# Kernel tuning notes

Hardware: AMD Instinct MI355X
Metric: run time of the kernel (lower is better)

Reference implementation:

```python
import math
import jax, jax.numpy as jnp
import numpy as np

B, S, D, H = 4, 1024, 1024, 16
DK = D // H
NEG = jnp.float32(-1e32)
EPS = 1e-5


def setup_inputs() -> dict:
    key = jax.random.key(0)
    ks = jax.random.split(key, 10)
    s = 1.0 / math.sqrt(D)
    return {
        "query": jax.random.normal(ks[0], (B, S, D), jnp.float32),
        "key": jax.random.normal(ks[1], (B, S, D), jnp.float32),
        "values": jax.random.normal(ks[2], (B, S, D), jnp.float32),
        "lens": jax.random.randint(ks[3], (B,), 0, S).astype(jnp.int32),
        "state_weight": jax.random.normal(ks[4], (1, H, S, S), jnp.float32),
        # params (kq_same=True -> k shares q_linear weights)
        "Wq": jax.random.normal(ks[5], (D, D), jnp.float32) * s,
        "bq": jnp.zeros((D,), jnp.float32),
        "Wv": jax.random.normal(ks[6], (D, D), jnp.float32) * s,
        "bv": jnp.zeros((D,), jnp.float32),
        "Wo": jax.random.normal(ks[7], (D, D), jnp.float32) * s,
        "bo": jnp.zeros((D,), jnp.float32),
        "gamma": jnp.ones((D,), jnp.float32),
        "beta": jnp.zeros((D,), jnp.float32),
    }


def reference(query, key, values, lens, state_weight, Wq, bq, Wv, bv, Wo, bo, gamma, beta):
    # eval-mode forward of DTransformerLayer (peek_cur=False -> strictly causal)
    b, s, d = query.shape
    mask = jnp.tril(jnp.ones((s, s), bool), -1)[None, None]  # [1,1,S,S]

    q = (query @ Wq + bq).reshape(b, s, H, DK).transpose(0, 2, 1, 3)   # bhsd
    k = (key @ Wq + bq).reshape(b, s, H, DK).transpose(0, 2, 1, 3)     # shared weights (kq_same)
    v = (values @ Wv + bv).reshape(b, s, H, DK).transpose(0, 2, 1, 3)

    scores = jnp.einsum('bhqd,bhkd->bhqk', q, k) / math.sqrt(DK)
    scores = jnp.where(mask, scores, NEG)
    scores = jnp.where(mask, scores + state_weight, NEG)
    attn = jax.nn.softmax(scores, axis=-1)
    attn = jnp.where(mask, attn, 0.0)  # fully-masked rows (row 0) -> zeros, matching torch

    ctx = jnp.einsum('bhqk,bhkd->bhqd', attn, v).transpose(0, 2, 1, 3).reshape(b, s, d)
    out = ctx @ Wo + bo

    x = query + out  # dropout is identity in eval
    mu = jnp.mean(x, axis=-1, keepdims=True)
    var = jnp.mean(jnp.square(x - mu), axis=-1, keepdims=True)
    return (x - mu) * jax.lax.rsqrt(var + EPS) * gamma + beta
```

## Files before the change

kernel.cpp:

```cpp
#include <hip/hip_runtime.h>

#define B_ 4
#define S_ 1024
#define D_ 1024
#define H_ 16
#define DK_ 64

typedef __attribute__((ext_vector_type(8))) short short8;
typedef __attribute__((ext_vector_type(4))) float f32x4;
typedef __attribute__((ext_vector_type(16))) float f32x16;

static __device__ __forceinline__ unsigned bf16rne(float x) {
    unsigned b = __float_as_uint(x);
    return (b + 0x7FFFu + ((b >> 16) & 1u)) >> 16;
}

__global__ __launch_bounds__(256) void cvt3_bf16(
    const float* __restrict__ q, const float* __restrict__ k,
    const float* __restrict__ v, ushort* __restrict__ out)
{
    const size_t i = ((size_t)blockIdx.x * 256 + threadIdx.x) * 8;
    const size_t FM = (size_t)4 * 1024 * 1024;
    const float* in = (i < FM) ? q : (i < 2 * FM) ? k : v;
    const size_t off = i & (FM - 1);
    const float4 a = *reinterpret_cast<const float4*>(in + off);
    const float4 b = *reinterpret_cast<const float4*>(in + off + 4);
    union { ushort u[8]; int4 vv; } p;
    p.u[0] = (ushort)bf16rne(a.x); p.u[1] = (ushort)bf16rne(a.y);
    p.u[2] = (ushort)bf16rne(a.z); p.u[3] = (ushort)bf16rne(a.w);
    p.u[4] = (ushort)bf16rne(b.x); p.u[5] = (ushort)bf16rne(b.y);
    p.u[6] = (ushort)bf16rne(b.z); p.u[7] = (ushort)bf16rne(b.w);
    *reinterpret_cast<int4*>(out + i) = p.vv;
}

__global__ __launch_bounds__(256) void transpose_cvt3(
    const float* __restrict__ W0, const float* __restrict__ W1,
    const float* __restrict__ W2, ushort* __restrict__ T0,
    ushort* __restrict__ T1, ushort* __restrict__ T2)
{
    __shared__ float ts[32][33];
    const float* W = (blockIdx.z == 0) ? W0 : (blockIdx.z == 1) ? W1 : W2;
    ushort*     Wt = (blockIdx.z == 0) ? T0 : (blockIdx.z == 1) ? T1 : T2;
    const int t  = threadIdx.x;
    const int k0 = blockIdx.y * 32, n0 = blockIdx.x * 32;
    const int r  = t >> 3, c4 = (t & 7) * 4;
    const float4 v = *reinterpret_cast<const float4*>(&W[(size_t)(k0 + r) * 1024 + n0 + c4]);
    ts[r][c4] = v.x; ts[r][c4 + 1] = v.y; ts[r][c4 + 2] = v.z; ts[r][c4 + 3] = v.w;
    __syncthreads();
    ushort4 o;
    o.x = (ushort)bf16rne(ts[c4    ][r]);
    o.y = (ushort)bf16rne(ts[c4 + 1][r]);
    o.z = (ushort)bf16rne(ts[c4 + 2][r]);
    o.w = (ushort)bf16rne(ts[c4 + 3][r]);
    *reinterpret_cast<ushort4*>(&Wt[(size_t)(n0 + r) * 1024 + k0 + c4]) = o;
}

template<int MODE>
__global__ __launch_bounds__(256) void gemm_mfma(
    const ushort* __restrict__ X, const ushort* __restrict__ Wt,
    const float* __restrict__ bias, const float* __restrict__ resid,
    void* __restrict__ out0, void* __restrict__ out1)
{
    __shared__ ushort As[64 * 64];
    __shared__ ushort Bs[128 * 64];

    const int t    = threadIdx.x;
    const int lane = t & 63;
    const int w    = t >> 6;

    const int cpx     = gridDim.x >> 3;
    const int logical = (blockIdx.x & 7) * cpx + (blockIdx.x >> 3);
    const int bm = logical >> 3;
    const int bn = logical & 7;

    const int srow   = lane >> 3;
    const int schunk = (lane & 7) ^ srow;
    const ushort* ag[2];
    const ushort* bg[4];
#pragma unroll
    for (int j = 0; j < 2; ++j)
        ag[j] = X  + (size_t)(bm * 64 + (j * 4 + w) * 8 + srow) * 1024 + schunk * 8;
#pragma unroll
    for (int j = 0; j < 4; ++j)
        bg[j] = Wt + (size_t)(bn * 128 + (j * 4 + w) * 8 + srow) * 1024 + schunk * 8;

#define STAGE(k0)                                                                \
    do {                                                                         \
        _Pragma("unroll")                                                        \
        for (int j = 0; j < 2; ++j)                                              \
            __builtin_amdgcn_global_load_lds(                                    \
                (__attribute__((address_space(1))) const void*)(ag[j] + (k0)),   \
                (__attribute__((address_space(3))) void*)&As[(j * 4 + w) * 512], \
                16, 0, 0);                                                       \
        _Pragma("unroll")                                                        \
        for (int j = 0; j < 4; ++j)                                              \
            __builtin_amdgcn_global_load_lds(                                    \
                (__attribute__((address_space(1))) const void*)(bg[j] + (k0)),   \
                (__attribute__((address_space(3))) void*)&Bs[(j * 4 + w) * 512], \
                16, 0, 0);                                                       \
    } while (0)

    const int fr = lane & 15;
    const int fk = lane >> 4;
    const int wm = w >> 1, wn = w & 1;

    f32x4 acc[2][4];
#pragma unroll
    for (int m = 0; m < 2; ++m)
#pragma unroll
        for (int n = 0; n < 4; ++n) acc[m][n] = (f32x4){0.f, 0.f, 0.f, 0.f};

#pragma unroll 1
    for (int kt = 0; kt < 16; ++kt) {
        STAGE(kt * 64);
        __syncthreads();
#pragma unroll
        for (int ks = 0; ks < 2; ++ks) {
            short8 af[2], bf[4];
#pragma unroll
            for (int m = 0; m < 2; ++m) {
                const int row = wm * 32 + m * 16 + fr;
                af[m] = *reinterpret_cast<const short8*>(
                    &As[row * 64 + (((ks * 4 + fk) ^ (row & 7)) * 8)]);
            }
#pragma unroll
            for (int n = 0; n < 4; ++n) {
                const int row = wn * 64 + n * 16 + fr;
                bf[n] = *reinterpret_cast<const short8*>(
                    &Bs[row * 64 + (((ks * 4 + fk) ^ (row & 7)) * 8)]);
            }
#pragma unroll
            for (int m = 0; m < 2; ++m)
#pragma unroll
                for (int n = 0; n < 4; ++n)
                    acc[m][n] = __builtin_amdgcn_mfma_f32_16x16x32_bf16(
                        af[m], bf[n], acc[m][n], 0, 0, 0);
        }
        __syncthreads();
    }
#undef STAGE

#pragma unroll
    for (int m = 0; m < 2; ++m) {
        const int row0 = bm * 64 + wm * 32 + m * 16 + fk * 4;
#pragma unroll
        for (int n = 0; n < 4; ++n) {
            const int col = bn * 128 + wn * 64 + n * 16 + fr;
            const float bc = bias[col];
            if (MODE == 0) {
                float* o = (float*)out0;
#pragma unroll
                for (int j = 0; j < 4; ++j) {
                    const int row = row0 + j;
                    o[(size_t)row * 1024 + col] =
                        acc[m][n][j] + bc + resid[(size_t)row * 1024 + col];
                }
            } else if (MODE == 1) {
                ushort* o = (row0 < 4096) ? (ushort*)out0 : (ushort*)out1;
                const int r0 = row0 & 4095;
                const int b_ = r0 >> 10, s0 = r0 & 1023;
                const int h  = col >> 6,  dk = col & 63;
#pragma unroll
                for (int j = 0; j < 4; ++j)
                    o[(((size_t)b_ * H_ + h) * S_ + s0 + j) * DK_ + dk] =
                        (ushort)bf16rne(acc[m][n][j] + bc);
            } else {
                ushort* o = (ushort*)out0;
                const int b_ = row0 >> 10, s0 = row0 & 1023;
                const int h  = col >> 6,   dk = col & 63;
                ushort4 pk;
                pk.x = (ushort)bf16rne(acc[m][n][0] + bc);
                pk.y = (ushort)bf16rne(acc[m][n][1] + bc);
                pk.z = (ushort)bf16rne(acc[m][n][2] + bc);
                pk.w = (ushort)bf16rne(acc[m][n][3] + bc);
                *reinterpret_cast<ushort4*>(
                    &o[(((size_t)b_ * H_ + h) * DK_ + dk) * S_ + s0]) = pk;
            }
        }
    }
}

__global__ __launch_bounds__(256) void attn_mfma(
    const ushort* __restrict__ Qh, const ushort* __restrict__ Kh,
    const ushort* __restrict__ Vt, const float* __restrict__ SW,
    ushort* __restrict__ ctxP, float2* __restrict__ ml)
{
    __shared__ ushort Ks[2][4096];
    __shared__ ushort Vs[2][4096];

    const int t    = threadIdx.x;
    const int lane = t & 63;
    const int w    = t >> 6;
    const int bid  = blockIdx.x;
    const int bh   = bid & 63;
    const int b    = bh >> 4;
    const int h    = bh & 15;
    const int qp   = bid >> 6;
    const int p    = qp >> 3;
    int qb = qp & 7;
    qb = (qb < 4) ? qb : 11 - qb;

    const int ql = lane & 31;
    const int hi = lane >> 5;
    const int qrow = qb * 128 + ql * 4 + w;
    const int t0 = p * (qb + 1);
    const int nt = qb + 1;

    const ushort* Kg  = Kh + (size_t)bh * S_ * DK_;
    const ushort* Vg  = Vt + (size_t)bh * DK_ * S_;
    const float*  swp = SW + ((size_t)h * S_ + qrow) * S_;

    const ushort* kgp[2];
    const ushort* vgp[2];
#pragma unroll
    for (int j = 0; j < 2; ++j) {
        const int bb = w * 2 + j;
        const int g = bb >> 2, c = bb & 3;
        kgp[j] = Kg + (size_t)(g * 32 + ql) * DK_ + c * 16 + hi * 8;
        vgp[j] = Vg + (size_t)(g * 32 + ql) * S_  + c * 16 + hi * 8;
    }

#define ASTAGE(buf, k0)                                                          \
    do {                                                                         \
        _Pragma("unroll")                                                        \
        for (int j = 0; j < 2; ++j) {                                            \
            const int bb = w * 2 + j;                                            \
            __builtin_amdgcn_global_load_lds(                                    \
                (__attribute__((address_space(1))) const void*)(kgp[j] + (size_t)(k0) * DK_), \
                (__attribute__((address_space(3))) void*)&Ks[buf][bb * 512],     \
                16, 0, 0);                                                       \
            __builtin_amdgcn_global_load_lds(                                    \
                (__attribute__((address_space(1))) const void*)(vgp[j] + (k0)),  \
                (__attribute__((address_space(3))) void*)&Vs[buf][bb * 512],     \
                16, 0, 0);                                                       \
        }                                                                        \
    } while (0)

    short8 qf[4];
    {
        const ushort* Qg = Qh + ((size_t)bh * S_ + qrow) * DK_;
#pragma unroll
        for (int c = 0; c < 4; ++c) {
            union { int4 i; short8 s; } u;
            u.i = *reinterpret_cast<const int4*>(&Qg[c * 16 + hi * 8]);
            qf[c] = u.s;
        }
    }

    f32x16 accA, accB;
#pragma unroll
    for (int r = 0; r < 16; ++r) { accA[r] = 0.f; accB[r] = 0.f; }
    float mrow = -1e30f, lrow = 0.f;

    ASTAGE(0, t0 * 64);

#pragma unroll 1
    for (int kt = 0; kt < nt; ++kt) {
        const int cur = kt & 1;
        const int k0  = (t0 + kt) * 64;
        if (kt + 1 < nt) {
            ASTAGE(cur ^ 1, (t0 + kt + 1) * 64);
            asm volatile("s_waitcnt vmcnt(4)" ::: "memory");
        } else {
            asm volatile("s_waitcnt vmcnt(0)" ::: "memory");
        }
        __builtin_amdgcn_s_barrier();
        __builtin_amdgcn_sched_barrier(0);

        f32x16 sc[2];
#pragma unroll
        for (int g = 0; g < 2; ++g) {
#pragma unroll
            for (int r = 0; r < 16; ++r) sc[g][r] = 0.f;
#pragma unroll
            for (int c = 0; c < 4; ++c) {
                const short8 kf = *reinterpret_cast<const short8*>(
                    &Ks[cur][((g * 4 + c) * 64 + lane) * 8]);
                sc[g] = __builtin_amdgcn_mfma_f32_32x32x16_bf16(kf, qf[c], sc[g], 0, 0, 0);
            }
        }

        float swv[2][16];
#pragma unroll
        for (int g = 0; g < 2; ++g)
#pragma unroll
            for (int j = 0; j < 4; ++j) {
                const float4 v = *reinterpret_cast<const float4*>(
                    &swp[k0 + g * 32 + hi * 4 + j * 8]);
                swv[g][j * 4 + 0] = v.x; swv[g][j * 4 + 1] = v.y;
                swv[g][j * 4 + 2] = v.z; swv[g][j * 4 + 3] = v.w;
            }

        float pr[2][16];
        float tmax = -1e30f;
#pragma unroll
        for (int g = 0; g < 2; ++g)
#pragma unroll
            for (int r = 0; r < 16; ++r) {
                const int key = k0 + g * 32 + (r & 3) + ((r >> 2) << 3) + (hi << 2);
                const float s = (key < qrow) ? sc[g][r] * 0.125f + swv[g][r] : -1e30f;
                pr[g][r] = s;
                tmax = fmaxf(tmax, s);
            }
        tmax = fmaxf(tmax, __shfl_xor(tmax, 32, 64));
        const float mnew = fmaxf(mrow, tmax);
        const float corr = __expf(mrow - mnew);
        float psum = 0.f;
#pragma unroll
        for (int g = 0; g < 2; ++g)
#pragma unroll
            for (int r = 0; r < 16; ++r) {
                const float e = (pr[g][r] > -1e29f) ? __expf(pr[g][r] - mnew) : 0.f;
                pr[g][r] = e;
                psum += e;
            }
        psum += __shfl_xor(psum, 32, 64);
        lrow = lrow * corr + psum;
        mrow = mnew;
#pragma unroll
        for (int r = 0; r < 16; ++r) { accA[r] *= corr; accB[r] *= corr; }

        short8 paf[4];
#pragma unroll
        for (int g = 0; g < 2; ++g) {
            unsigned pk[8];
#pragma unroll
            for (int j = 0; j < 8; ++j)
                pk[j] = bf16rne(pr[g][2 * j]) | (bf16rne(pr[g][2 * j + 1]) << 16);
            unsigned x0 = (unsigned)__shfl_xor((int)pk[0], 32, 64);
            unsigned x1 = (unsigned)__shfl_xor((int)pk[1], 32, 64);
            unsigned x2 = (unsigned)__shfl_xor((int)pk[2], 32, 64);
            unsigned x3 = (unsigned)__shfl_xor((int)pk[3], 32, 64);
            unsigned x4 = (unsigned)__shfl_xor((int)pk[4], 32, 64);
            unsigned x5 = (unsigned)__shfl_xor((int)pk[5], 32, 64);
            unsigned x6 = (unsigned)__shfl_xor((int)pk[6], 32, 64);
            unsigned x7 = (unsigned)__shfl_xor((int)pk[7], 32, 64);
            union { unsigned u[4]; short8 s; } a0, a1;
            a0.u[0] = hi ? x2 : pk[0];
            a0.u[1] = hi ? x3 : pk[1];
            a0.u[2] = hi ? pk[2] : x0;
            a0.u[3] = hi ? pk[3] : x1;
            a1.u[0] = hi ? x6 : pk[4];
            a1.u[1] = hi ? x7 : pk[5];
            a1.u[2] = hi ? pk[6] : x4;
            a1.u[3] = hi ? pk[7] : x5;
            paf[g * 2 + 0] = a0.s;
            paf[g * 2 + 1] = a1.s;
        }

#pragma unroll
        for (int cc = 0; cc < 4; ++cc) {
            const short8 va = *reinterpret_cast<const short8*>(
                &Vs[cur][((0 * 4 + cc) * 64 + lane) * 8]);
            const short8 vb = *reinterpret_cast<const short8*>(
                &Vs[cur][((1 * 4 + cc) * 64 + lane) * 8]);
            accA = __builtin_amdgcn_mfma_f32_32x32x16_bf16(va, paf[cc], accA, 0, 0, 0);
            accB = __builtin_amdgcn_mfma_f32_32x32x16_bf16(vb, paf[cc], accB, 0, 0, 0);
        }

        __builtin_amdgcn_sched_barrier(0);
        __builtin_amdgcn_s_barrier();
        __builtin_amdgcn_sched_barrier(0);
    }
#undef ASTAGE

    const float inv = (lrow > 0.f) ? 1.f / lrow : 0.f;
    ushort* crow_ = ctxP + (size_t)p * 4194304 +
                    ((size_t)b * S_ + qrow) * D_ + h * DK_;
#pragma unroll
    for (int g = 0; g < 4; ++g) {
        ushort4 oA, oB;
        oA.x = (ushort)bf16rne(accA[4 * g + 0] * inv);
        oA.y = (ushort)bf16rne(accA[4 * g + 1] * inv);
        oA.z = (ushort)bf16rne(accA[4 * g + 2] * inv);
        oA.w = (ushort)bf16rne(accA[4 * g + 3] * inv);
        oB.x = (ushort)bf16rne(accB[4 * g + 0] * inv);
        oB.y = (ushort)bf16rne(accB[4 * g + 1] * inv);
        oB.z = (ushort)bf16rne(accB[4 * g + 2] * inv);
        oB.w = (ushort)bf16rne(accB[4 * g + 3] * inv);
        *reinterpret_cast<ushort4*>(&crow_[g * 8 + hi * 4])      = oA;
        *reinterpret_cast<ushort4*>(&crow_[g * 8 + hi * 4 + 32]) = oB;
    }
    if (hi == 0) {
        float2 v; v.x = mrow; v.y = lrow;
        ml[((size_t)p * 64 + bh) * 1024 + qrow] = v;
    }
}

__global__ __launch_bounds__(256) void attn_merge(
    const ushort* __restrict__ ctxP, const float2* __restrict__ ml,
    ushort* __restrict__ ctx)
{
    const size_t idx = ((size_t)blockIdx.x * 256 + threadIdx.x) * 8;
    const int col = (int)(idx & 1023);
    const int row = (int)(idx >> 10);
    const int b = row >> 10, s = row & 1023;
    const int h = col >> 6;
    const int bh = b * 16 + h;
    const float2 ml0 = ml[(size_t)bh * 1024 + s];
    const float2 ml1 = ml[(size_t)(64 + bh) * 1024 + s];
    const float m  = fmaxf(ml0.x, ml1.x);
    const float a0 = ml0.y * __expf(ml0.x - m);
    const float a1 = ml1.y * __expf(ml1.x - m);
    const float d  = a0 + a1;
    const float w0 = (d > 0.f) ? a0 / d : 0.f;
    const float w1 = (d > 0.f) ? a1 / d : 0.f;
    union { int4 v; ushort u[8]; } p0, p1, o;
    p0.v = *reinterpret_cast<const int4*>(ctxP + idx);
    p1.v = *reinterpret_cast<const int4*>(ctxP + 4194304 + idx);
#pragma unroll
    for (int i = 0; i < 8; ++i) {
        const float f0 = __uint_as_float((unsigned)p0.u[i] << 16);
        const float f1 = __uint_as_float((unsigned)p1.u[i] << 16);
        o.u[i] = (ushort)bf16rne(w0 * f0 + w1 * f1);
    }
    *reinterpret_cast<int4*>(ctx + idx) = o.v;
}

__global__ __launch_bounds__(256) void layernorm_k(
    const float* __restrict__ x, const float* __restrict__ gamma,
    const float* __restrict__ beta, float* __restrict__ out)
{
    const int row = blockIdx.x;
    const int t   = threadIdx.x;
    const float4 v = *reinterpret_cast<const float4*>(&x[(size_t)row * D_ + (t << 2)]);
    float sum = v.x + v.y + v.z + v.w;
    float sq  = v.x * v.x + v.y * v.y + v.z * v.z + v.w * v.w;
#pragma unroll
    for (int w = 1; w < 64; w <<= 1) {
        sum += __shfl_xor(sum, w, 64);
        sq  += __shfl_xor(sq,  w, 64);
    }
    __shared__ float red[8];
    const int wid = t >> 6;
    if ((t & 63) == 0) { red[wid] = sum; red[wid + 4] = sq; }
    __syncthreads();
    sum = red[0] + red[1] + red[2] + red[3];
    sq  = red[4] + red[5] + red[6] + red[7];
    const float mu  = sum * (1.f / 1024.f);
    const float var = sq * (1.f / 1024.f) - mu * mu;
    const float rs  = rsqrtf(var + 1e-5f);
    const float4 gm = *reinterpret_cast<const float4*>(&gamma[t << 2]);
    const float4 bt = *reinterpret_cast<const float4*>(&beta[t << 2]);
    float4 o;
    o.x = (v.x - mu) * rs * gm.x + bt.x;
    o.y = (v.y - mu) * rs * gm.y + bt.y;
    o.z = (v.z - mu) * rs * gm.z + bt.z;
    o.w = (v.w - mu) * rs * gm.w + bt.w;
    *reinterpret_cast<float4*>(&out[(size_t)row * D_ + (t << 2)]) = o;
}

extern "C" void kernel_launch(void* const* d_in, const int* in_sizes, int n_in,
                              void* d_out, int out_size, void* d_ws, size_t ws_size,
                              hipStream_t stream)
{
    const float* query  = (const float*)d_in[0];
    const float* key    = (const float*)d_in[1];
    const float* values = (const float*)d_in[2];
    const float* SW     = (const float*)d_in[4];
    const float* Wq     = (const float*)d_in[5];
    const float* bq     = (const float*)d_in[6];
    const float* Wv     = (const float*)d_in[7];
    const float* bv     = (const float*)d_in[8];
    const float* Wo     = (const float*)d_in[9];
    const float* bo     = (const float*)d_in[10];
    const float* gamma  = (const float*)d_in[11];
    const float* beta   = (const float*)d_in[12];

    char* ws = (char*)d_ws;
    const size_t MB = 1024 * 1024;
    ushort* qbf  = (ushort*)(ws);
    ushort* kbf  = (ushort*)(ws +  8 * MB);
    ushort* vbf  = (ushort*)(ws + 16 * MB);
    ushort* Wqt  = (ushort*)(ws + 24 * MB);
    ushort* Wvt  = (ushort*)(ws + 26 * MB);
    ushort* Wot  = (ushort*)(ws + 28 * MB);
    ushort* Qh   = (ushort*)(ws + 30 * MB);
    ushort* Kh   = (ushort*)(ws + 38 * MB);
    ushort* Vt   = (ushort*)(ws + 46 * MB);
    float2* ml   = (float2*)(ws + 54 * MB);
    ushort* ctxP = qbf;
    ushort* ctxm = vbf;
    float*  xbf  = (float*)(ws + 30 * MB);

    const dim3 blk(256);

    cvt3_bf16<<<dim3(6144), blk, 0, stream>>>(query, key, values, qbf);
    transpose_cvt3<<<dim3(32, 32, 3), blk, 0, stream>>>(Wq, Wv, Wo, Wqt, Wvt, Wot);

    gemm_mfma<1><<<dim3(1024), blk, 0, stream>>>(qbf, Wqt, bq, nullptr, Qh, Kh);
    gemm_mfma<2><<<dim3(512),  blk, 0, stream>>>(vbf, Wvt, bv, nullptr, Vt, nullptr);

    attn_mfma<<<dim3(1024), blk, 0, stream>>>(Qh, Kh, Vt, SW, ctxP, ml);
    attn_merge<<<dim3(2048), blk, 0, stream>>>(ctxP, ml, ctxm);

    gemm_mfma<0><<<dim3(512), blk, 0, stream>>>(ctxm, Wot, bo, query, xbf, nullptr);

    layernorm_k<<<dim3(4096), blk, 0, stream>>>(xbf, gamma, beta, (float*)d_out);
}
```

Before: 144.2 us.

## Double-buffer GEMM loads, rebalance attention key-splits, skip masking on interior tiles

The GEMM main loop gets double-buffered LDS staging: the next K tile loads while the current one is consumed, with explicit vmcnt waits, raw barriers, and raised wave priority around the MFMAs. Attention replaces the fixed two-way key split with variable-size chunks of up to four tiles, giving 1280 evenly sized blocks plus an XCD-aware block remap. The causal-mask compare is skipped on tiles lying entirely below the diagonal, and the probability pack uses v_cvt_pk_bf16_f32. The merge kernel now combines up to four partial results per row through a compact chunk layout, and workspace buffers are shuffled to fit.

```diff
diff --git a/kernel.cpp b/kernel.cpp
--- a/kernel.cpp
+++ b/kernel.cpp
@@ -9,6 +9,8 @@
 typedef __attribute__((ext_vector_type(8))) short short8;
 typedef __attribute__((ext_vector_type(4))) float f32x4;
 typedef __attribute__((ext_vector_type(16))) float f32x16;
+
+#define CBASE_PACK 0x100C090604020100ULL
 
 static __device__ __forceinline__ unsigned bf16rne(float x) {
     unsigned b = __float_as_uint(x);
@@ -61,8 +63,8 @@
     const float* __restrict__ bias, const float* __restrict__ resid,
     void* __restrict__ out0, void* __restrict__ out1)
 {
-    __shared__ ushort As[64 * 64];
-    __shared__ ushort Bs[128 * 64];
+    __shared__ ushort As[2][64 * 64];
+    __shared__ ushort Bs[2][128 * 64];
 
     const int t    = threadIdx.x;
     const int lane = t & 63;
@@ -84,19 +86,19 @@
     for (int j = 0; j < 4; ++j)
         bg[j] = Wt + (size_t)(bn * 128 + (j * 4 + w) * 8 + srow) * 1024 + schunk * 8;
 
-#define STAGE(k0)                                                                \
+#define STAGE(buf, k0)                                                           \
     do {                                                                         \
         _Pragma("unroll")                                                        \
         for (int j = 0; j < 2; ++j)                                              \
             __builtin_amdgcn_global_load_lds(                                    \
                 (__attribute__((address_space(1))) const void*)(ag[j] + (k0)),   \
-                (__attribute__((address_space(3))) void*)&As[(j * 4 + w) * 512], \
+                (__attribute__((address_space(3))) void*)&As[buf][(j * 4 + w) * 512], \
                 16, 0, 0);                                                       \
         _Pragma("unroll")                                                        \
         for (int j = 0; j < 4; ++j)                                              \
             __builtin_amdgcn_global_load_lds(                                    \
                 (__attribute__((address_space(1))) const void*)(bg[j] + (k0)),   \
-                (__attribute__((address_space(3))) void*)&Bs[(j * 4 + w) * 512], \
+                (__attribute__((address_space(3))) void*)&Bs[buf][(j * 4 + w) * 512], \
                 16, 0, 0);                                                       \
     } while (0)
 
@@ -110,10 +112,18 @@
 #pragma unroll
         for (int n = 0; n < 4; ++n) acc[m][n] = (f32x4){0.f, 0.f, 0.f, 0.f};
 
+    STAGE(0, 0);
 #pragma unroll 1
     for (int kt = 0; kt < 16; ++kt) {
-        STAGE(kt * 64);
-        __syncthreads();
+        const int cur = kt & 1;
+        if (kt + 1 < 16) {
+            STAGE(cur ^ 1, (kt + 1) * 64);
+            asm volatile("s_waitcnt vmcnt(6)" ::: "memory");
+        } else {
+            asm volatile("s_waitcnt vmcnt(0)" ::: "memory");
+        }
+        __builtin_amdgcn_s_barrier();
+        __builtin_amdgcn_sched_barrier(0);
 #pragma unroll
         for (int ks = 0; ks < 2; ++ks) {
             short8 af[2], bf[4];
@@ -121,22 +131,26 @@
             for (int m = 0; m < 2; ++m) {
                 const int row = wm * 32 + m * 16 + fr;
                 af[m] = *reinterpret_cast<const short8*>(
-                    &As[row * 64 + (((ks * 4 + fk) ^ (row & 7)) * 8)]);
+                    &As[cur][row * 64 + (((ks * 4 + fk) ^ (row & 7)) * 8)]);
             }
 #pragma unroll
             for (int n = 0; n < 4; ++n) {
                 const int row = wn * 64 + n * 16 + fr;
                 bf[n] = *reinterpret_cast<const short8*>(
-                    &Bs[row * 64 + (((ks * 4 + fk) ^ (row & 7)) * 8)]);
-            }
+                    &Bs[cur][row * 64 + (((ks * 4 + fk) ^ (row & 7)) * 8)]);
+            }
+            __builtin_amdgcn_s_setprio(1);
 #pragma unroll
             for (int m = 0; m < 2; ++m)
 #pragma unroll
                 for (int n = 0; n < 4; ++n)
                     acc[m][n] = __builtin_amdgcn_mfma_f32_16x16x32_bf16(
                         af[m], bf[n], acc[m][n], 0, 0, 0);
-        }
-        __syncthreads();
+            __builtin_amdgcn_s_setprio(0);
+        }
+        __builtin_amdgcn_sched_barrier(0);
+        __builtin_amdgcn_s_barrier();
+        __builtin_amdgcn_sched_barrier(0);
     }
 #undef STAGE
 
@@ -191,20 +205,22 @@
     const int t    = threadIdx.x;
     const int lane = t & 63;
     const int w    = t >> 6;
-    const int bid  = blockIdx.x;
-    const int bh   = bid & 63;
-    const int b    = bh >> 4;
-    const int h    = bh & 15;
-    const int qp   = bid >> 6;
-    const int p    = qp >> 3;
-    int qb = qp & 7;
-    qb = (qb < 4) ? qb : 11 - qb;
+    const int lg = (blockIdx.x & 7) * 160 + (blockIdx.x >> 3);
+    const int bh = lg / 20;
+    const int ci = lg - bh * 20;
+    const int b  = bh >> 4;
+    const int h  = bh & 15;
+    int qb = 0;
+#pragma unroll
+    for (int q = 1; q < 8; ++q)
+        if ((int)((CBASE_PACK >> (q * 8)) & 0xff) <= ci) qb = q;
+    const int lc = ci - (int)((CBASE_PACK >> (qb * 8)) & 0xff);
+    const int t0 = lc * 4;
+    const int nt = min(4, 2 * qb + 2 - t0);
 
     const int ql = lane & 31;
     const int hi = lane >> 5;
     const int qrow = qb * 128 + ql * 4 + w;
-    const int t0 = p * (qb + 1);
-    const int nt = qb + 1;
 
     const ushort* Kg  = Kh + (size_t)bh * S_ * DK_;
     const ushort* Vg  = Vt + (size_t)bh * DK_ * S_;
@@ -268,6 +284,7 @@
         __builtin_amdgcn_sched_barrier(0);
 
         f32x16 sc[2];
+        __builtin_amdgcn_s_setprio(1);
 #pragma unroll
         for (int g = 0; g < 2; ++g) {
 #pragma unroll
@@ -279,6 +296,7 @@
                 sc[g] = __builtin_amdgcn_mfma_f32_32x32x16_bf16(kf, qf[c], sc[g], 0, 0, 0);
             }
         }
+        __builtin_amdgcn_s_setprio(0);
 
         float swv[2][16];
 #pragma unroll
@@ -293,15 +311,26 @@
 
         float pr[2][16];
         float tmax = -1e30f;
-#pragma unroll
-        for (int g = 0; g < 2; ++g)
-#pragma unroll
-            for (int r = 0; r < 16; ++r) {
-                const int key = k0 + g * 32 + (r & 3) + ((r >> 2) << 3) + (hi << 2);
-                const float s = (key < qrow) ? sc[g][r] * 0.125f + swv[g][r] : -1e30f;
-                pr[g][r] = s;
-                tmax = fmaxf(tmax, s);
-            }
+        if (t0 + kt >= 2 * qb) {
+#pragma unroll
+            for (int g = 0; g < 2; ++g)
+#pragma unroll
+                for (int r = 0; r < 16; ++r) {
+                    const int key = k0 + g * 32 + (r & 3) + ((r >> 2) << 3) + (hi << 2);
+                    const float s = (key < qrow) ? sc[g][r] * 0.125f + swv[g][r] : -1e30f;
+                    pr[g][r] = s;
+                    tmax = fmaxf(tmax, s);
+                }
+        } else {
+#pragma unroll
+            for (int g = 0; g < 2; ++g)
+#pragma unroll
+                for (int r = 0; r < 16; ++r) {
+                    const float s = sc[g][r] * 0.125f + swv[g][r];
+                    pr[g][r] = s;
+                    tmax = fmaxf(tmax, s);
+                }
+        }
         tmax = fmaxf(tmax, __shfl_xor(tmax, 32, 64));
         const float mnew = fmaxf(mrow, tmax);
         const float corr = __expf(mrow - mnew);
@@ -325,8 +354,12 @@
         for (int g = 0; g < 2; ++g) {
             unsigned pk[8];
 #pragma unroll
-            for (int j = 0; j < 8; ++j)
-                pk[j] = bf16rne(pr[g][2 * j]) | (bf16rne(pr[g][2 * j + 1]) << 16);
+            for (int j = 0; j < 8; ++j) {
+                unsigned r_;
+                asm("v_cvt_pk_bf16_f32 %0, %1, %2"
+                    : "=v"(r_) : "v"(pr[g][2 * j]), "v"(pr[g][2 * j + 1]));
+                pk[j] = r_;
+            }
             unsigned x0 = (unsigned)__shfl_xor((int)pk[0], 32, 64);
             unsigned x1 = (unsigned)__shfl_xor((int)pk[1], 32, 64);
             unsigned x2 = (unsigned)__shfl_xor((int)pk[2], 32, 64);
@@ -348,6 +381,7 @@
             paf[g * 2 + 1] = a1.s;
         }
 
+        __builtin_amdgcn_s_setprio(1);
 #pragma unroll
         for (int cc = 0; cc < 4; ++cc) {
             const short8 va = *reinterpret_cast<const short8*>(
@@ -357,6 +391,7 @@
             accA = __builtin_amdgcn_mfma_f32_32x32x16_bf16(va, paf[cc], accA, 0, 0, 0);
             accB = __builtin_amdgcn_mfma_f32_32x32x16_bf16(vb, paf[cc], accB, 0, 0, 0);
         }
+        __builtin_amdgcn_s_setprio(0);
 
         __builtin_amdgcn_sched_barrier(0);
         __builtin_amdgcn_s_barrier();
@@ -365,8 +400,7 @@
 #undef ASTAGE
 
     const float inv = (lrow > 0.f) ? 1.f / lrow : 0.f;
-    ushort* crow_ = ctxP + (size_t)p * 4194304 +
-                    ((size_t)b * S_ + qrow) * D_ + h * DK_;
+    ushort* crow_ = ctxP + ((size_t)(bh * 20 + ci) * 128 + (ql * 4 + w)) * 64;
 #pragma unroll
     for (int g = 0; g < 4; ++g) {
         ushort4 oA, oB;
@@ -383,7 +417,7 @@
     }
     if (hi == 0) {
         float2 v; v.x = mrow; v.y = lrow;
-        ml[((size_t)p * 64 + bh) * 1024 + qrow] = v;
+        ml[(size_t)(bh * 20 + ci) * 128 + ql * 4 + w] = v;
     }
 }
 
@@ -395,26 +429,43 @@
     const int col = (int)(idx & 1023);
     const int row = (int)(idx >> 10);
     const int b = row >> 10, s = row & 1023;
-    const int h = col >> 6;
+    const int h = col >> 6, dk0 = col & 63;
     const int bh = b * 16 + h;
-    const float2 ml0 = ml[(size_t)bh * 1024 + s];
-    const float2 ml1 = ml[(size_t)(64 + bh) * 1024 + s];
-    const float m  = fmaxf(ml0.x, ml1.x);
-    const float a0 = ml0.y * __expf(ml0.x - m);
-    const float a1 = ml1.y * __expf(ml1.x - m);
-    const float d  = a0 + a1;
-    const float w0 = (d > 0.f) ? a0 / d : 0.f;
-    const float w1 = (d > 0.f) ? a1 / d : 0.f;
-    union { int4 v; ushort u[8]; } p0, p1, o;
-    p0.v = *reinterpret_cast<const int4*>(ctxP + idx);
-    p1.v = *reinterpret_cast<const int4*>(ctxP + 4194304 + idx);
-#pragma unroll
-    for (int i = 0; i < 8; ++i) {
-        const float f0 = __uint_as_float((unsigned)p0.u[i] << 16);
-        const float f1 = __uint_as_float((unsigned)p1.u[i] << 16);
-        o.u[i] = (ushort)bf16rne(w0 * f0 + w1 * f1);
-    }
-    *reinterpret_cast<int4*>(ctx + idx) = o.v;
+    const int qb = s >> 7, rl = s & 127;
+    const int nch = (qb + 2) >> 1;
+    const int cb  = (int)((CBASE_PACK >> (qb * 8)) & 0xff);
+
+    float mm[4], ll[4];
+    float m = -1e30f;
+#pragma unroll
+    for (int c = 0; c < 4; ++c)
+        if (c < nch) {
+            const float2 v = ml[(size_t)(bh * 20 + cb + c) * 128 + rl];
+            mm[c] = v.x; ll[c] = v.y;
+            m = fmaxf(m, v.x);
+        }
+    float wc[4], wsum = 0.f;
+#pragma unroll
+    for (int c = 0; c < 4; ++c)
+        if (c < nch) { wc[c] = ll[c] * __expf(mm[c] - m); wsum += wc[c]; }
+    const float inv = (wsum > 0.f) ? 1.f / wsum : 0.f;
+
+    float o[8] = {0.f, 0.f, 0.f, 0.f, 0.f, 0.f, 0.f, 0.f};
+#pragma unroll
+    for (int c = 0; c < 4; ++c)
+        if (c < nch) {
+            union { int4 v; ushort u[8]; } p;
+            p.v = *reinterpret_cast<const int4*>(
+                &ctxP[((size_t)(bh * 20 + cb + c) * 128 + rl) * 64 + dk0]);
+            const float wgt = wc[c] * inv;
+#pragma unroll
+            for (int i = 0; i < 8; ++i)
+                o[i] += wgt * __uint_as_float((unsigned)p.u[i] << 16);
+        }
+    union { int4 v; ushort u[8]; } r;
+#pragma unroll
+    for (int i = 0; i < 8; ++i) r.u[i] = (ushort)bf16rne(o[i]);
+    *reinterpret_cast<int4*>(ctx + idx) = r.v;
 }
 
 __global__ __launch_bounds__(256) void layernorm_k(
@@ -469,19 +520,19 @@
 
     char* ws = (char*)d_ws;
     const size_t MB = 1024 * 1024;
-    ushort* qbf  = (ushort*)(ws);
-    ushort* kbf  = (ushort*)(ws +  8 * MB);
-    ushort* vbf  = (ushort*)(ws + 16 * MB);
+    ushort* Qh   = (ushort*)(ws);
+    ushort* Kh   = (ushort*)(ws +  8 * MB);
+    ushort* Vt   = (ushort*)(ws + 16 * MB);
     ushort* Wqt  = (ushort*)(ws + 24 * MB);
     ushort* Wvt  = (ushort*)(ws + 26 * MB);
     ushort* Wot  = (ushort*)(ws + 28 * MB);
-    ushort* Qh   = (ushort*)(ws + 30 * MB);
-    ushort* Kh   = (ushort*)(ws + 38 * MB);
-    ushort* Vt   = (ushort*)(ws + 46 * MB);
+    ushort* qbf  = (ushort*)(ws + 30 * MB);
+    ushort* kbf  = (ushort*)(ws + 38 * MB);
+    ushort* vbf  = (ushort*)(ws + 46 * MB);
     float2* ml   = (float2*)(ws + 54 * MB);
     ushort* ctxP = qbf;
-    ushort* ctxm = vbf;
-    float*  xbf  = (float*)(ws + 30 * MB);
+    ushort* ctxm = Qh;
+    float*  xbf  = (float*)(ws + 8 * MB);
 
     const dim3 blk(256);
 
@@ -491,7 +542,7 @@
     gemm_mfma<1><<<dim3(1024), blk, 0, stream>>>(qbf, Wqt, bq, nullptr, Qh, Kh);
     gemm_mfma<2><<<dim3(512),  blk, 0, stream>>>(vbf, Wvt, bv, nullptr, Vt, nullptr);
 
-    attn_mfma<<<dim3(1024), blk, 0, stream>>>(Qh, Kh, Vt, SW, ctxP, ml);
+    attn_mfma<<<dim3(1280), blk, 0, stream>>>(Qh, Kh, Vt, SW, ctxP, ml);
     attn_merge<<<dim3(2048), blk, 0, stream>>>(ctxP, ml, ctxm);
 
     gemm_mfma<0><<<dim3(512), blk, 0, stream>>>(ctxm, Wot, bo, query, xbf, nullptr);
```

New measurement: 148.1 us. 1.03x slower.
